# Performance work log

Measured on AMD Instinct MI355X. Metric: run time of the kernel, lower is better.

The kernel has to match this reference:

```python
import jax, jax.numpy as jnp
import numpy as np

B, T = 64, 512
VOCAB, E, H = 20, 64, 128
D = 2 * H            # 256, bidirectional LSTM output dim
NH, KD = 8, D // 8   # 8 heads, key_dim 32
DU, OUT = 256, 128
NEG = -1e9


def _lstm_scan(x, mask, W, U, b):
    # x: [B,T,E], mask: [B,T] bool. Keras gate order: i, f, g(c), o.
    Bb = x.shape[0]
    Hh = U.shape[0]
    def step(carry, inp):
        h, c = carry
        xt, mt = inp                      # [B,E], [B]
        z = xt @ W + h @ U + b            # [B,4H]
        i, f, g, o = jnp.split(z, 4, axis=-1)
        c_new = jax.nn.sigmoid(f) * c + jax.nn.sigmoid(i) * jnp.tanh(g)
        h_new = jax.nn.sigmoid(o) * jnp.tanh(c_new)
        m = mt[:, None]
        h = jnp.where(m, h_new, h)        # freeze state/output on masked steps
        c = jnp.where(m, c_new, c)
        return (h, c), h
    h0 = jnp.zeros((Bb, Hh), x.dtype)
    _, ys = jax.lax.scan(step, (h0, h0), (jnp.swapaxes(x, 0, 1), mask.T))
    return jnp.swapaxes(ys, 0, 1)         # [B,T,H]


def setup_inputs() -> dict:
    key = jax.random.key(0)
    ks = jax.random.split(key, 24)
    g = lambda k, shape, s: (jax.random.normal(k, shape, jnp.float32) * s)
    inp = {
        'sequences': jax.random.randint(ks[0], (B, T), 0, VOCAB),
        'emb': g(ks[1], (VOCAB, E), 0.05),
        # forward LSTM
        'Wf': g(ks[2], (E, 4 * H), 0.05), 'Uf': g(ks[3], (H, 4 * H), 0.05), 'bf': jnp.zeros((4 * H,), jnp.float32),
        # backward LSTM
        'Wb': g(ks[4], (E, 4 * H), 0.05), 'Ub': g(ks[5], (H, 4 * H), 0.05), 'bb': jnp.zeros((4 * H,), jnp.float32),
        # MHA projections
        'Wq': g(ks[6], (D, NH, KD), 0.05), 'bq': jnp.zeros((NH, KD), jnp.float32),
        'Wk': g(ks[7], (D, NH, KD), 0.05), 'bk': jnp.zeros((NH, KD), jnp.float32),
        'Wv': g(ks[8], (D, NH, KD), 0.05), 'bv': jnp.zeros((NH, KD), jnp.float32),
        'Wo': g(ks[9], (NH, KD, D), 0.05), 'bo': jnp.zeros((D,), jnp.float32),
        # MLP head (input is concat of avg+max pool -> 2*D)
        'W1': g(ks[10], (2 * D, DU), 0.05), 'b1': jnp.zeros((DU,), jnp.float32),
        'W2': g(ks[11], (DU, DU // 2), 0.05), 'b2': jnp.zeros((DU // 2,), jnp.float32),
        'W3': g(ks[12], (DU // 2, OUT), 0.05), 'b3': jnp.zeros((OUT,), jnp.float32),
    }
    return inp


def _forward(sequences, emb, Wf, Uf, bf, Wb, Ub, bb, Wq, bq, Wk, bk, Wv, bv, Wo, bo, W1, b1, W2, b2, W3, b3):
    mask = sequences != 0                       # mask_zero=True
    x = emb[sequences]                          # [B,T,E]
    fwd = _lstm_scan(x, mask, Wf, Uf, bf)
    bwd = _lstm_scan(x[:, ::-1], mask[:, ::-1], Wb, Ub, bb)[:, ::-1]
    h = jnp.concatenate([fwd, bwd], axis=-1)    # [B,T,D]
    # Multi-head self-attention (key-masked, Keras MHA math)
    q = jnp.einsum('btd,dhk->bthk', h, Wq) + bq
    k = jnp.einsum('btd,dhk->bthk', h, Wk) + bk
    v = jnp.einsum('btd,dhk->bthk', h, Wv) + bv
    scores = jnp.einsum('bthk,bshk->bhts', q, k) / jnp.sqrt(jnp.float32(KD))
    scores = jnp.where(mask[:, None, None, :], scores, NEG)
    attn = jax.nn.softmax(scores, axis=-1)      # [B,H,T,T]
    ctx = jnp.einsum('bhts,bshk->bthk', attn, v)
    att = jnp.einsum('bthk,hkd->btd', ctx, Wo) + bo   # [B,T,D]
    # dual pooling (masked mean + masked max)
    mf = mask[..., None].astype(att.dtype)
    avg = (att * mf).sum(axis=1) / jnp.maximum(mf.sum(axis=1), 1.0)
    mx = jnp.where(mask[..., None], att, NEG).max(axis=1)
    p = jnp.concatenate([avg, mx], axis=-1)     # [B,2D]
    x1 = jax.nn.relu(p @ W1 + b1)
    x2 = jax.nn.relu(x1 @ W2 + b2)
    return x2 @ W3 + b3                         # [B,OUT]


def reference(sequences, emb, Wf, Uf, bf, Wb, Ub, bb, Wq, bq, Wk, bk, Wv, bv, Wo, bo, W1, b1, W2, b2, W3, b3):
    return _forward(sequences, emb, Wf, Uf, bf, Wb, Ub, bb, Wq, bq, Wk, bk, Wv, bv, Wo, bo, W1, b1, W2, b2, W3, b3)
```

## Files before the change

kernel.cpp:

```cpp
#include <hip/hip_runtime.h>
#include <math.h>

#define B_ 64
#define T_ 512
#define E_ 64
#define H_ 128
#define NH_ 8
#define KD_ 32
#define BT_ (B_ * T_)
#define NEG_ -1e9f

__device__ __forceinline__ float sigmoidf_(float x) {
    return 1.f / (1.f + __expf(-x));
}
__device__ __forceinline__ float tanhf_(float x) {
    return 1.f - 2.f / (1.f + __expf(2.f * x));
}

__device__ __forceinline__ float qswap1(float x) {
    return __int_as_float(__builtin_amdgcn_mov_dpp(__float_as_int(x), 0xB1, 0xF, 0xF, true));
}
__device__ __forceinline__ float qswap2(float x) {
    return __int_as_float(__builtin_amdgcn_mov_dpp(__float_as_int(x), 0x4E, 0xF, 0xF, true));
}

template <bool GATHER, bool PERM>
__global__ __launch_bounds__(256, 3) void gemm_f32(
    const float* __restrict__ A, const int* __restrict__ gidx,
    const float* __restrict__ emb, const float* __restrict__ Bm,
    const float* __restrict__ bias, float* __restrict__ C,
    int M, int N, int K)
{
    __shared__ __align__(16) float As[16][132];
    __shared__ __align__(16) float Bs[16][128];
    const int tid = threadIdx.x;
    const int tx = tid & 15, ty = tid >> 4;
    const int ntn = N >> 7;
    const int bm = blockIdx.x / ntn, bn = blockIdx.x % ntn;
    const int m0 = bm << 7, n0 = bn << 7;

    float acc[8][8];
#pragma unroll
    for (int i = 0; i < 8; ++i)
#pragma unroll
        for (int j = 0; j < 8; ++j) acc[i][j] = 0.f;

    const int ac4 = (tid & 3) << 2;
    const int ar  = tid >> 2;
    const int bc4 = (tid & 31) << 2;
    const int br  = tid >> 5;

    for (int k0 = 0; k0 < K; k0 += 16) {
        __syncthreads();
#pragma unroll
        for (int p = 0; p < 2; ++p) {
            const int r = ar + p * 64;
            const int gm = m0 + r;
            const float* src = GATHER
                ? (emb + (size_t)gidx[gm] * K + (k0 + ac4))
                : (A + (size_t)gm * K + (k0 + ac4));
            float4 v = *(const float4*)src;
            As[ac4 + 0][r] = v.x; As[ac4 + 1][r] = v.y;
            As[ac4 + 2][r] = v.z; As[ac4 + 3][r] = v.w;
        }
#pragma unroll
        for (int p = 0; p < 2; ++p) {
            const int rr = br + p * 8;
            if (PERM) {
                const float* brow = Bm + (size_t)(k0 + rr) * N;
                const int base = (n0 >> 2) + (tid & 31);
                Bs[rr][bc4 + 0] = brow[base];
                Bs[rr][bc4 + 1] = brow[128 + base];
                Bs[rr][bc4 + 2] = brow[256 + base];
                Bs[rr][bc4 + 3] = brow[384 + base];
            } else {
                float4 v = *(const float4*)(Bm + (size_t)(k0 + rr) * N + (n0 + bc4));
                *(float4*)&Bs[rr][bc4] = v;
            }
        }
        __syncthreads();
#pragma unroll
        for (int k = 0; k < 16; ++k) {
            float a[8], b[8];
            *(float4*)&a[0] = *(const float4*)&As[k][ty << 3];
            *(float4*)&a[4] = *(const float4*)&As[k][(ty << 3) + 4];
            *(float4*)&b[0] = *(const float4*)&Bs[k][tx << 3];
            *(float4*)&b[4] = *(const float4*)&Bs[k][(tx << 3) + 4];
#pragma unroll
            for (int i = 0; i < 8; ++i)
#pragma unroll
                for (int j = 0; j < 8; ++j)
                    acc[i][j] = fmaf(a[i], b[j], acc[i][j]);
        }
    }

    float bv[8];
#pragma unroll
    for (int j = 0; j < 8; ++j) {
        const int n = n0 + (tx << 3) + j;
        bv[j] = PERM ? bias[((n & 3) << 7) + (n >> 2)] : bias[n];
    }
#pragma unroll
    for (int i = 0; i < 8; ++i) {
        float* dst = C + (size_t)(m0 + (ty << 3) + i) * N + n0 + (tx << 3);
        float4 o0 = { acc[i][0] + bv[0], acc[i][1] + bv[1],
                      acc[i][2] + bv[2], acc[i][3] + bv[3] };
        float4 o1 = { acc[i][4] + bv[4], acc[i][5] + bv[5],
                      acc[i][6] + bv[6], acc[i][7] + bv[7] };
        *(float4*)dst = o0;
        *(float4*)(dst + 4) = o1;
    }
}

__global__ __launch_bounds__(512, 2) void lstm_scan(
    const int* __restrict__ seq,
    const float* __restrict__ xwf, const float* __restrict__ xwb,
    const float* __restrict__ Uf, const float* __restrict__ Ub,
    float* __restrict__ hcat)
{
    const int w = blockIdx.x;
    const int dir = w & 1, b = w >> 1;
    const float* xw = dir ? xwb : xwf;
    const float* U  = dir ? Ub  : Uf;
    const int tid = threadIdx.x;
    const int jj = tid >> 2, ks = tid & 3;

    __shared__ __align__(16) float hbuf[2][4][36];
    __shared__ float mkl[T_];

    float u[4][32];
#pragma unroll
    for (int g = 0; g < 4; ++g)
#pragma unroll
        for (int kk = 0; kk < 32; ++kk)
            u[g][kk] = U[(size_t)(32 * ks + kk) * 512 + g * 128 + jj];
#pragma unroll
    for (int g = 0; g < 4; ++g)
#pragma unroll
        for (int kk = 0; kk < 32; ++kk)
            asm volatile("" : "+v"(u[g][kk]));

    mkl[tid] = (seq[b * T_ + tid] != 0) ? 1.f : 0.f;
    if (tid < 2 * 4 * 36) ((float*)hbuf)[tid] = 0.f;

    float h_cur = 0.f, c_cur = 0.f;
    float* ho = hcat + (size_t)b * T_ * 256 + dir * 128;
    const float* xr = xw + (size_t)b * T_ * 512;

    __syncthreads();

    int te = dir ? (T_ - 1) : 0;
    float4 xwv = *(const float4*)&xr[(size_t)te * 512 + jj * 4];

    int p = 0;
    for (int t = 0; t < T_; ++t) {
        const int te_n  = dir ? (te - 1) : (te + 1);
        const int te_pf = (t == T_ - 1) ? te : te_n;
        const float4 xw_n = *(const float4*)&xr[(size_t)te_pf * 512 + jj * 4];

        float a0 = 0.f, a1 = 0.f, a2 = 0.f, a3 = 0.f;
        const float* hc = hbuf[p][ks];
#pragma unroll
        for (int c = 0; c < 8; ++c) {
            const float4 h4 = *(const float4*)&hc[c * 4];
            a0 = fmaf(h4.x, u[0][c*4+0], a0); a0 = fmaf(h4.y, u[0][c*4+1], a0);
            a0 = fmaf(h4.z, u[0][c*4+2], a0); a0 = fmaf(h4.w, u[0][c*4+3], a0);
            a1 = fmaf(h4.x, u[1][c*4+0], a1); a1 = fmaf(h4.y, u[1][c*4+1], a1);
            a1 = fmaf(h4.z, u[1][c*4+2], a1); a1 = fmaf(h4.w, u[1][c*4+3], a1);
            a2 = fmaf(h4.x, u[2][c*4+0], a2); a2 = fmaf(h4.y, u[2][c*4+1], a2);
            a2 = fmaf(h4.z, u[2][c*4+2], a2); a2 = fmaf(h4.w, u[2][c*4+3], a2);
            a3 = fmaf(h4.x, u[3][c*4+0], a3); a3 = fmaf(h4.y, u[3][c*4+1], a3);
            a3 = fmaf(h4.z, u[3][c*4+2], a3); a3 = fmaf(h4.w, u[3][c*4+3], a3);
        }
        a0 += qswap1(a0); a0 += qswap2(a0);
        a1 += qswap1(a1); a1 += qswap2(a1);
        a2 += qswap1(a2); a2 += qswap2(a2);
        a3 += qswap1(a3); a3 += qswap2(a3);

        const float zi = xwv.x + a0, zf = xwv.y + a1;
        const float zg = xwv.z + a2, zo = xwv.w + a3;
        const float cn = fmaf(sigmoidf_(zf), c_cur, sigmoidf_(zi) * tanhf_(zg));
        const float hn = sigmoidf_(zo) * tanhf_(cn);
        const float m  = mkl[te];
        const float hm = (m > 0.5f) ? hn : h_cur;
        c_cur = (m > 0.5f) ? cn : c_cur;
        h_cur = hm;

        if ((jj >> 5) == ks) hbuf[1 - p][ks][jj & 31] = hm;
        if (ks == 0) ho[(size_t)te * 256 + jj] = hm;
        __syncthreads();
        p ^= 1; te = te_n; xwv = xw_n;
    }
}

__global__ __launch_bounds__(256, 2) void attn_fused(
    const int* __restrict__ seq,
    const float* __restrict__ q, const float* __restrict__ kk,
    const float* __restrict__ vv, float* __restrict__ ctx)
{
    const int wg = blockIdx.x;
    const int b = wg >> 3, h = wg & 7;
    const int tid = threadIdx.x;

    __shared__ __align__(16) float Ks[16][32];
    __shared__ __align__(16) float Vs[16][32];
    __shared__ float mk[16];

    float qA[32], qB[32];
    {
        const float* qp  = q + (((size_t)(b * T_) + tid) * NH_ + h) * KD_;
        const float* qp2 = qp + (size_t)256 * NH_ * KD_;
#pragma unroll
        for (int k = 0; k < 32; k += 4) {
            float4 v0 = *(const float4*)(qp + k);
            float4 v1 = *(const float4*)(qp2 + k);
            qA[k] = v0.x; qA[k + 1] = v0.y; qA[k + 2] = v0.z; qA[k + 3] = v0.w;
            qB[k] = v1.x; qB[k + 1] = v1.y; qB[k + 2] = v1.z; qB[k + 3] = v1.w;
        }
    }
    float ctxA[32], ctxB[32];
#pragma unroll
    for (int k = 0; k < 32; ++k) { ctxA[k] = 0.f; ctxB[k] = 0.f; }
    float mA = -1e30f, mB = -1e30f, lA = 0.f, lB = 0.f;

    const int lr = (tid & 127) >> 3;
    const int lc = (tid & 7) << 2;
    const bool loadV = (tid >= 128);

    for (int c = 0; c < T_ / 16; ++c) {
        const int s0 = c << 4;
        __syncthreads();
        {
            const float* src = (loadV ? vv : kk) +
                (((size_t)(b * T_) + s0 + lr) * NH_ + h) * KD_ + lc;
            float4 v = *(const float4*)src;
            if (loadV) *(float4*)&Vs[lr][lc] = v;
            else       *(float4*)&Ks[lr][lc] = v;
            if (tid < 16) mk[tid] = (seq[b * T_ + s0 + tid] != 0) ? 0.f : 1.f;
        }
        __syncthreads();

        float sA[16], sB[16];
#pragma unroll
        for (int s = 0; s < 16; ++s) {
            float dA = 0.f, dB = 0.f;
#pragma unroll
            for (int k = 0; k < 32; k += 4) {
                float4 k4 = *(const float4*)&Ks[s][k];
                dA = fmaf(k4.x, qA[k], dA); dA = fmaf(k4.y, qA[k + 1], dA);
                dA = fmaf(k4.z, qA[k + 2], dA); dA = fmaf(k4.w, qA[k + 3], dA);
                dB = fmaf(k4.x, qB[k], dB); dB = fmaf(k4.y, qB[k + 1], dB);
                dB = fmaf(k4.z, qB[k + 2], dB); dB = fmaf(k4.w, qB[k + 3], dB);
            }
            const float SCL = 0.17677669529663687f;
            const bool masked = (mk[s] > 0.5f);
            sA[s] = masked ? NEG_ : dA * SCL;
            sB[s] = masked ? NEG_ : dB * SCL;
        }
        float cmA = sA[0], cmB = sB[0];
#pragma unroll
        for (int s = 1; s < 16; ++s) {
            cmA = fmaxf(cmA, sA[s]); cmB = fmaxf(cmB, sB[s]);
        }
        const float mnA = fmaxf(mA, cmA), mnB = fmaxf(mB, cmB);
        const float alA = __expf(mA - mnA), alB = __expf(mB - mnB);
        float psA = 0.f, psB = 0.f;
#pragma unroll
        for (int s = 0; s < 16; ++s) {
            float pa = __expf(sA[s] - mnA); sA[s] = pa; psA += pa;
            float pb = __expf(sB[s] - mnB); sB[s] = pb; psB += pb;
        }
        lA = fmaf(lA, alA, psA); lB = fmaf(lB, alB, psB);
        mA = mnA; mB = mnB;
#pragma unroll
        for (int k = 0; k < 32; ++k) { ctxA[k] *= alA; ctxB[k] *= alB; }
#pragma unroll
        for (int s = 0; s < 16; ++s) {
#pragma unroll
            for (int k = 0; k < 32; k += 4) {
                float4 v4 = *(const float4*)&Vs[s][k];
                ctxA[k]     = fmaf(sA[s], v4.x, ctxA[k]);
                ctxA[k + 1] = fmaf(sA[s], v4.y, ctxA[k + 1]);
                ctxA[k + 2] = fmaf(sA[s], v4.z, ctxA[k + 2]);
                ctxA[k + 3] = fmaf(sA[s], v4.w, ctxA[k + 3]);
                ctxB[k]     = fmaf(sB[s], v4.x, ctxB[k]);
                ctxB[k + 1] = fmaf(sB[s], v4.y, ctxB[k + 1]);
                ctxB[k + 2] = fmaf(sB[s], v4.z, ctxB[k + 2]);
                ctxB[k + 3] = fmaf(sB[s], v4.w, ctxB[k + 3]);
            }
        }
    }

    const float iA = 1.f / lA, iB = 1.f / lB;
    float* dA_ = ctx + (((size_t)(b * T_) + tid) * NH_ + h) * KD_;
    float* dB_ = dA_ + (size_t)256 * NH_ * KD_;
#pragma unroll
    for (int k = 0; k < 32; k += 4) {
        float4 o0 = { ctxA[k] * iA, ctxA[k + 1] * iA,
                      ctxA[k + 2] * iA, ctxA[k + 3] * iA };
        float4 o1 = { ctxB[k] * iB, ctxB[k + 1] * iB,
                      ctxB[k + 2] * iB, ctxB[k + 3] * iB };
        *(float4*)(dA_ + k) = o0;
        *(float4*)(dB_ + k) = o1;
    }
}

__global__ void pool_kernel(const int* __restrict__ seq,
                            const float* __restrict__ att,
                            float* __restrict__ p)
{
    const int b = blockIdx.x;
    const int d = threadIdx.x;
    __shared__ float mk[T_];
    for (int t = d; t < T_; t += 256)
        mk[t] = (seq[b * T_ + t] != 0) ? 1.f : 0.f;
    __syncthreads();
    float sum = 0.f, mx = NEG_, cnt = 0.f;
    for (int t = 0; t < T_; ++t) {
        const float a = att[((size_t)b * T_ + t) * 256 + d];
        const float m = mk[t];
        cnt += m;
        sum = fmaf(m, a, sum);
        mx = fmaxf(mx, (m > 0.5f) ? a : NEG_);
    }
    p[b * 512 + d] = sum / fmaxf(cnt, 1.f);
    p[b * 512 + 256 + d] = mx;
}

__global__ void mlp_kernel(const float* __restrict__ p,
                           const float* __restrict__ W1, const float* __restrict__ b1,
                           const float* __restrict__ W2, const float* __restrict__ b2,
                           const float* __restrict__ W3, const float* __restrict__ b3,
                           float* __restrict__ out)
{
    const int b = blockIdx.x;
    const int tid = threadIdx.x;
    __shared__ float pl[512];
    __shared__ float x1l[256];
    __shared__ float x2l[128];
    pl[tid] = p[b * 512 + tid];
    pl[tid + 256] = p[b * 512 + 256 + tid];
    __syncthreads();
    {
        float acc = b1[tid];
        for (int k = 0; k < 512; ++k) acc = fmaf(pl[k], W1[k * 256 + tid], acc);
        x1l[tid] = fmaxf(acc, 0.f);
    }
    __syncthreads();
    if (tid < 128) {
        float acc = b2[tid];
        for (int k = 0; k < 256; ++k) acc = fmaf(x1l[k], W2[k * 128 + tid], acc);
        x2l[tid] = fmaxf(acc, 0.f);
    }
    __syncthreads();
    if (tid < 128) {
        float acc = b3[tid];
        for (int k = 0; k < 128; ++k) acc = fmaf(x2l[k], W3[k * 128 + tid], acc);
        out[b * 128 + tid] = acc;
    }
}

extern "C" void kernel_launch(void* const* d_in, const int* in_sizes, int n_in,
                              void* d_out, int out_size, void* d_ws, size_t ws_size,
                              hipStream_t stream)
{
    (void)in_sizes; (void)n_in; (void)out_size; (void)ws_size;
    const int*   seq = (const int*)d_in[0];
    const float* emb = (const float*)d_in[1];
    const float* Wf  = (const float*)d_in[2];
    const float* Uf  = (const float*)d_in[3];
    const float* bf  = (const float*)d_in[4];
    const float* Wb  = (const float*)d_in[5];
    const float* Ub  = (const float*)d_in[6];
    const float* bb  = (const float*)d_in[7];
    const float* Wq  = (const float*)d_in[8];
    const float* bq  = (const float*)d_in[9];
    const float* Wk  = (const float*)d_in[10];
    const float* bk  = (const float*)d_in[11];
    const float* Wv  = (const float*)d_in[12];
    const float* bv  = (const float*)d_in[13];
    const float* Wo  = (const float*)d_in[14];
    const float* bo  = (const float*)d_in[15];
    const float* W1  = (const float*)d_in[16];
    const float* b1  = (const float*)d_in[17];
    const float* W2  = (const float*)d_in[18];
    const float* b2  = (const float*)d_in[19];
    const float* W3  = (const float*)d_in[20];
    const float* b3  = (const float*)d_in[21];
    float* out = (float*)d_out;
    float* ws  = (float*)d_ws;

    float* xw_f = ws;
    float* xw_b = ws + 16777216;
    float* hcat = ws + 33554432;
    float* qb   = ws;
    float* kb   = ws + 8388608;
    float* vb   = ws + 16777216;
    float* cxb  = ws + 25165824;
    float* attb = ws + 33554432;
    float* pb   = ws + 41943040;

    const dim3 blk256(256), blk512(512);

    gemm_f32<true, true><<<dim3((BT_ / 128) * (512 / 128)), blk256, 0, stream>>>(
        nullptr, seq, emb, Wf, bf, xw_f, BT_, 512, 64);
    gemm_f32<true, true><<<dim3((BT_ / 128) * (512 / 128)), blk256, 0, stream>>>(
        nullptr, seq, emb, Wb, bb, xw_b, BT_, 512, 64);

    lstm_scan<<<dim3(128), blk512, 0, stream>>>(seq, xw_f, xw_b, Uf, Ub, hcat);

    gemm_f32<false, false><<<dim3((BT_ / 128) * (256 / 128)), blk256, 0, stream>>>(
        hcat, nullptr, nullptr, Wq, bq, qb, BT_, 256, 256);
    gemm_f32<false, false><<<dim3((BT_ / 128) * (256 / 128)), blk256, 0, stream>>>(
        hcat, nullptr, nullptr, Wk, bk, kb, BT_, 256, 256);
    gemm_f32<false, false><<<dim3((BT_ / 128) * (256 / 128)), blk256, 0, stream>>>(
        hcat, nullptr, nullptr, Wv, bv, vb, BT_, 256, 256);

    attn_fused<<<dim3(B_ * NH_), blk256, 0, stream>>>(seq, qb, kb, vb, cxb);

    gemm_f32<false, false><<<dim3((BT_ / 128) * (256 / 128)), blk256, 0, stream>>>(
        cxb, nullptr, nullptr, Wo, bo, attb, BT_, 256, 256);

    pool_kernel<<<dim3(B_), blk256, 0, stream>>>(seq, attb, pb);
    mlp_kernel<<<dim3(B_), blk256, 0, stream>>>(pb, W1, b1, W2, b2, W3, b3, out);
}
```

Baseline: 985.8 us.

## Use split-bf16 MFMA GEMMs for QKV and output projections

Replaces the fp32 SIMT GEMMs for the Q/K/V and output projections with a matrix-core kernel. Each operand is split into high and low bf16 parts and three MFMA products are summed, keeping close to fp32 accuracy. The LSTM and attention kernels now write their outputs directly as bf16 hi/lo pairs, and small kernels convert and transpose the weights on every call. The LSTM launch bounds change and the asm register-pinning of U is removed, which risks register spills or lower occupancy in the serial scan, where most of the time is likely spent.

Measured after the change: 911.4 us. 1.08x faster.

```diff
diff --git a/kernel.cpp b/kernel.cpp
--- a/kernel.cpp
+++ b/kernel.cpp
@@ -10,11 +10,29 @@
 #define BT_ (B_ * T_)
 #define NEG_ -1e9f
 
+typedef __attribute__((ext_vector_type(8))) short bf16x8_t;
+typedef __attribute__((ext_vector_type(4))) float f32x4_t;
+typedef unsigned short ushort_t;
+typedef unsigned int uint_t;
+
 __device__ __forceinline__ float sigmoidf_(float x) {
     return 1.f / (1.f + __expf(-x));
 }
 __device__ __forceinline__ float tanhf_(float x) {
     return 1.f - 2.f / (1.f + __expf(2.f * x));
+}
+
+__device__ __forceinline__ ushort_t bf16_rne(float x) {
+    uint_t u = __float_as_uint(x);
+    uint_t r = (u + 0x7FFFu + ((u >> 16) & 1u)) >> 16;
+    return (ushort_t)r;
+}
+__device__ __forceinline__ float bf16_to_f(ushort_t h) {
+    return __uint_as_float(((uint_t)h) << 16);
+}
+__device__ __forceinline__ void split_bf16(float x, ushort_t& h, ushort_t& l) {
+    h = bf16_rne(x);
+    l = bf16_rne(x - bf16_to_f(h));
 }
 
 __device__ __forceinline__ float qswap1(float x) {
@@ -112,11 +130,110 @@
     }
 }
 
-__global__ __launch_bounds__(512, 2) void lstm_scan(
+__global__ void wconv(const float* __restrict__ W,
+                      ushort_t* __restrict__ Bh, ushort_t* __restrict__ Bl)
+{
+    const int k = blockIdx.x, n = threadIdx.x;
+    float v = W[k * 256 + n];
+    ushort_t h, l;
+    split_bf16(v, h, l);
+    Bh[n * 256 + k] = h;
+    Bl[n * 256 + k] = l;
+}
+
+__global__ __launch_bounds__(256, 2) void gemm_mfma3(
+    const ushort_t* __restrict__ Ah, const ushort_t* __restrict__ Al,
+    const ushort_t* __restrict__ Bh, const ushort_t* __restrict__ Bl,
+    const float* __restrict__ bias, float* __restrict__ C,
+    int M, int N)
+{
+    __shared__ __align__(16) ushort_t Alds[2][128 * 40];
+    __shared__ __align__(16) ushort_t Blds[2][128 * 40];
+
+    const int tid = threadIdx.x;
+    const int ntn = N >> 7;
+    const int bm = blockIdx.x / ntn, bn = blockIdx.x % ntn;
+    const int m0 = bm << 7, n0 = bn << 7;
+
+    const int w = tid >> 6;
+    const int wr = w >> 1, wc = w & 1;
+    const int lane = tid & 63;
+    const int fr = lane & 15, kg = lane >> 4;
+
+    const int sr = tid >> 1;
+    const int sh = (tid & 1) << 4;
+
+    f32x4_t acc[4][4];
+#pragma unroll
+    for (int i = 0; i < 4; ++i)
+#pragma unroll
+        for (int j = 0; j < 4; ++j) acc[i][j] = (f32x4_t){0.f, 0.f, 0.f, 0.f};
+
+    for (int ks = 0; ks < 8; ++ks) {
+        const int k0 = ks << 5;
+        __syncthreads();
+        {
+            const size_t ga = (size_t)(m0 + sr) * 256 + k0 + sh;
+            const size_t gb = (size_t)(n0 + sr) * 256 + k0 + sh;
+            const int ld = sr * 40 + sh;
+            const uint4* pah = (const uint4*)(Ah + ga);
+            const uint4* pal = (const uint4*)(Al + ga);
+            const uint4* pbh = (const uint4*)(Bh + gb);
+            const uint4* pbl = (const uint4*)(Bl + gb);
+            uint4* qah = (uint4*)&Alds[0][ld];
+            uint4* qal = (uint4*)&Alds[1][ld];
+            uint4* qbh = (uint4*)&Blds[0][ld];
+            uint4* qbl = (uint4*)&Blds[1][ld];
+            qah[0] = pah[0]; qah[1] = pah[1];
+            qal[0] = pal[0]; qal[1] = pal[1];
+            qbh[0] = pbh[0]; qbh[1] = pbh[1];
+            qbl[0] = pbl[0]; qbl[1] = pbl[1];
+        }
+        __syncthreads();
+
+        bf16x8_t ah[4], al[4], bh[4], bl[4];
+#pragma unroll
+        for (int i = 0; i < 4; ++i) {
+            const int ra = (wr * 64 + i * 16 + fr) * 40 + kg * 8;
+            const int rb = (wc * 64 + i * 16 + fr) * 40 + kg * 8;
+            ah[i] = *(const bf16x8_t*)&Alds[0][ra];
+            al[i] = *(const bf16x8_t*)&Alds[1][ra];
+            bh[i] = *(const bf16x8_t*)&Blds[0][rb];
+            bl[i] = *(const bf16x8_t*)&Blds[1][rb];
+        }
+#pragma unroll
+        for (int i = 0; i < 4; ++i)
+#pragma unroll
+            for (int j = 0; j < 4; ++j) {
+                acc[i][j] = __builtin_amdgcn_mfma_f32_16x16x32_bf16(
+                    ah[i], bh[j], acc[i][j], 0, 0, 0);
+                acc[i][j] = __builtin_amdgcn_mfma_f32_16x16x32_bf16(
+                    ah[i], bl[j], acc[i][j], 0, 0, 0);
+                acc[i][j] = __builtin_amdgcn_mfma_f32_16x16x32_bf16(
+                    al[i], bh[j], acc[i][j], 0, 0, 0);
+            }
+    }
+
+#pragma unroll
+    for (int j = 0; j < 4; ++j) {
+        const int col = n0 + wc * 64 + j * 16 + fr;
+        const float bv = bias[col];
+#pragma unroll
+        for (int i = 0; i < 4; ++i) {
+#pragma unroll
+            for (int r = 0; r < 4; ++r) {
+                const int row = m0 + wr * 64 + i * 16 + kg * 4 + r;
+                C[(size_t)row * N + col] = acc[i][j][r] + bv;
+            }
+        }
+    }
+}
+
+__global__ __launch_bounds__(512, 1) void lstm_scan(
     const int* __restrict__ seq,
     const float* __restrict__ xwf, const float* __restrict__ xwb,
     const float* __restrict__ Uf, const float* __restrict__ Ub,
-    float* __restrict__ hcat)
+    ushort_t* __restrict__ hch, ushort_t* __restrict__ hcl)
 {
     const int w = blockIdx.x;
     const int dir = w & 1, b = w >> 1;
@@ -134,17 +251,13 @@
 #pragma unroll
         for (int kk = 0; kk < 32; ++kk)
             u[g][kk] = U[(size_t)(32 * ks + kk) * 512 + g * 128 + jj];
-#pragma unroll
-    for (int g = 0; g < 4; ++g)
-#pragma unroll
-        for (int kk = 0; kk < 32; ++kk)
-            asm volatile("" : "+v"(u[g][kk]));
 
     mkl[tid] = (seq[b * T_ + tid] != 0) ? 1.f : 0.f;
     if (tid < 2 * 4 * 36) ((float*)hbuf)[tid] = 0.f;
 
     float h_cur = 0.f, c_cur = 0.f;
-    float* ho = hcat + (size_t)b * T_ * 256 + dir * 128;
+    ushort_t* hoh = hch + (size_t)b * T_ * 256 + dir * 128;
+    ushort_t* hol = hcl + (size_t)b * T_ * 256 + dir * 128;
     const float* xr = xw + (size_t)b * T_ * 512;
 
     __syncthreads();
@@ -187,7 +300,12 @@
         h_cur = hm;
 
         if ((jj >> 5) == ks) hbuf[1 - p][ks][jj & 31] = hm;
-        if (ks == 0) ho[(size_t)te * 256 + jj] = hm;
+        if (ks == 0) {
+            ushort_t hh, hl;
+            split_bf16(hm, hh, hl);
+            hoh[(size_t)te * 256 + jj] = hh;
+            hol[(size_t)te * 256 + jj] = hl;
+        }
         __syncthreads();
         p ^= 1; te = te_n; xwv = xw_n;
     }
@@ -196,7 +314,8 @@
 __global__ __launch_bounds__(256, 2) void attn_fused(
     const int* __restrict__ seq,
     const float* __restrict__ q, const float* __restrict__ kk,
-    const float* __restrict__ vv, float* __restrict__ ctx)
+    const float* __restrict__ vv,
+    ushort_t* __restrict__ cxh, ushort_t* __restrict__ cxl)
 {
     const int wg = blockIdx.x;
     const int b = wg >> 3, h = wg & 7;
@@ -292,16 +411,17 @@
     }
 
     const float iA = 1.f / lA, iB = 1.f / lB;
-    float* dA_ = ctx + (((size_t)(b * T_) + tid) * NH_ + h) * KD_;
-    float* dB_ = dA_ + (size_t)256 * NH_ * KD_;
-#pragma unroll
-    for (int k = 0; k < 32; k += 4) {
-        float4 o0 = { ctxA[k] * iA, ctxA[k + 1] * iA,
-                      ctxA[k + 2] * iA, ctxA[k + 3] * iA };
-        float4 o1 = { ctxB[k] * iB, ctxB[k + 1] * iB,
-                      ctxB[k + 2] * iB, ctxB[k + 3] * iB };
-        *(float4*)(dA_ + k) = o0;
-        *(float4*)(dB_ + k) = o1;
+    ushort_t* chA = cxh + (((size_t)(b * T_) + tid) * NH_ + h) * KD_;
+    ushort_t* clA = cxl + (((size_t)(b * T_) + tid) * NH_ + h) * KD_;
+    ushort_t* chB = chA + (size_t)256 * NH_ * KD_;
+    ushort_t* clB = clA + (size_t)256 * NH_ * KD_;
+#pragma unroll
+    for (int k = 0; k < 32; ++k) {
+        ushort_t hA, lA_, hB, lB_;
+        split_bf16(ctxA[k] * iA, hA, lA_);
+        split_bf16(ctxB[k] * iB, hB, lB_);
+        chA[k] = hA; clA[k] = lA_;
+        chB[k] = hB; clB[k] = lB_;
     }
 }
 
@@ -392,34 +512,46 @@
 
     float* xw_f = ws;
     float* xw_b = ws + 16777216;
-    float* hcat = ws + 33554432;
     float* qb   = ws;
     float* kb   = ws + 8388608;
     float* vb   = ws + 16777216;
-    float* cxb  = ws + 25165824;
+    ushort_t* cxh = (ushort_t*)(ws + 25165824);
+    ushort_t* cxl = cxh + (size_t)BT_ * 256;
+    ushort_t* hch = (ushort_t*)(ws + 33554432);
+    ushort_t* hcl = hch + (size_t)BT_ * 256;
     float* attb = ws + 33554432;
     float* pb   = ws + 41943040;
+    ushort_t* wt = (ushort_t*)(ws + 41975808);
+    ushort_t* Wqh = wt + 0 * 65536, *Wql = wt + 1 * 65536;
+    ushort_t* Wkh = wt + 2 * 65536, *Wkl = wt + 3 * 65536;
+    ushort_t* Wvh = wt + 4 * 65536, *Wvl = wt + 5 * 65536;
+    ushort_t* Woh = wt + 6 * 65536, *Wol = wt + 7 * 65536;
 
     const dim3 blk256(256), blk512(512);
+
+    wconv<<<dim3(256), blk256, 0, stream>>>(Wq, Wqh, Wql);
+    wconv<<<dim3(256), blk256, 0, stream>>>(Wk, Wkh, Wkl);
+    wconv<<<dim3(256), blk256, 0, stream>>>(Wv, Wvh, Wvl);
+    wconv<<<dim3(256), blk256, 0, stream>>>(Wo, Woh, Wol);
 
     gemm_f32<true, true><<<dim3((BT_ / 128) * (512 / 128)), blk256, 0, stream>>>(
         nullptr, seq, emb, Wf, bf, xw_f, BT_, 512, 64);
     gemm_f32<true, true><<<dim3((BT_ / 128) * (512 / 128)), blk256, 0, stream>>>(
         nullptr, seq, emb, Wb, bb, xw_b, BT_, 512, 64);
 
-    lstm_scan<<<dim3(128), blk512, 0, stream>>>(seq, xw_f, xw_b, Uf, Ub, hcat);
-
-    gemm_f32<false, false><<<dim3((BT_ / 128) * (256 / 128)), blk256, 0, stream>>>(
-        hcat, nullptr, nullptr, Wq, bq, qb, BT_, 256, 256);
-    gemm_f32<false, false><<<dim3((BT_ / 128) * (256 / 128)), blk256, 0, stream>>>(
-        hcat, nullptr, nullptr, Wk, bk, kb, BT_, 256, 256);
-    gemm_f32<false, false><<<dim3((BT_ / 128) * (256 / 128)), blk256, 0, stream>>>(
-        hcat, nullptr, nullptr, Wv, bv, vb, BT_, 256, 256);
-
-    attn_fused<<<dim3(B_ * NH_), blk256, 0, stream>>>(seq, qb, kb, vb, cxb);
-
-    gemm_f32<false, false><<<dim3((BT_ / 128) * (256 / 128)), blk256, 0, stream>>>(
-        cxb, nullptr, nullptr, Wo, bo, attb, BT_, 256, 256);
+    lstm_scan<<<dim3(128), blk512, 0, stream>>>(seq, xw_f, xw_b, Uf, Ub, hch, hcl);
+
+    gemm_mfma3<<<dim3((BT_ / 128) * 2), blk256, 0, stream>>>(
+        hch, hcl, Wqh, Wql, bq, qb, BT_, 256);
+    gemm_mfma3<<<dim3((BT_ / 128) * 2), blk256, 0, stream>>>(
+        hch, hcl, Wkh, Wkl, bk, kb, BT_, 256);
+    gemm_mfma3<<<dim3((BT_ / 128) * 2), blk256, 0, stream>>>(
+        hch, hcl, Wvh, Wvl, bv, vb, BT_, 256);
+
+    attn_fused<<<dim3(B_ * NH_), blk256, 0, stream>>>(seq, qb, kb, vb, cxh, cxl);
+
+    gemm_mfma3<<<dim3((BT_ / 128) * 2), blk256, 0, stream>>>(
+        cxh, cxl, Woh, Wol, bo, attb, BT_, 256);
 
     pool_kernel<<<dim3(B_), blk256, 0, stream>>>(seq, attb, pb);
     mlp_kernel<<<dim3(B_), blk256, 0, stream>>>(pb, W1, b1, W2, b2, W3, b3, out);
```
